# Kernel optimization log

Measured on AMD Instinct MI355X. Metric: run time of the kernel, lower is better.

## Reference

```python
import jax, jax.numpy as jnp
import numpy as np

TEMPERATURE = 0.1
LOSS_SCALE = 1.0
LAMBD = 0.5


def setup_inputs() -> dict:
    key = jax.random.key(0)
    k1, k2 = jax.random.split(key)
    B, D = 4096, 768
    predicted = jax.random.normal(k1, (B, D), dtype=jnp.float32)
    target = jax.random.normal(k2, (B, D), dtype=jnp.float32)
    return {"predicted": predicted, "target": target}


def reference(predicted, target):
    predicted = predicted.astype(jnp.float32)
    target = target.astype(jnp.float32)
    B = predicted.shape[0]

    # Pairwise L2 distances via Gram identity (avoids B x B x D intermediate):
    # ||p_i - t_j||^2 = ||p_i||^2 + ||t_j||^2 - 2 p_i . t_j
    p_sq = jnp.sum(predicted * predicted, axis=-1)  # [B]
    t_sq = jnp.sum(target * target, axis=-1)        # [B]
    cross = predicted @ target.T                    # [B, B]
    sq_dist = p_sq[:, None] + t_sq[None, :] - 2.0 * cross
    distances = jnp.sqrt(jnp.maximum(sq_dist, 0.0))  # [B, B]

    logits = -distances / TEMPERATURE
    # cross-entropy with labels = arange(B): mean of -log_softmax diagonal
    log_probs = jax.nn.log_softmax(logits, axis=-1)
    contrastive_dist_loss = -jnp.mean(jnp.diagonal(log_probs))

    # normalized L1 magnitude loss
    elementwise_l1 = jnp.sum(jnp.abs(predicted - target), axis=-1)  # [B]
    target_magnitude = jnp.sum(jnp.abs(target), axis=-1)            # [B]
    norm_factor = jax.lax.stop_gradient(target_magnitude)
    normalized_magnitude_loss = jnp.mean(elementwise_l1 / norm_factor)

    total_loss = LOSS_SCALE * (
        LAMBD * contrastive_dist_loss + (1.0 - LAMBD) * normalized_magnitude_loss
    )
    return (total_loss, contrastive_dist_loss, normalized_magnitude_loss)
```

## Files before the change

### kernel.cpp

```cpp
#include <hip/hip_runtime.h>
#include <hip/hip_bf16.h>
#include <math.h>

#define B_ROWS 4096
#define D_DIM  768

#define BM 128
#define BN 256
#define BK 32
#define NKT (D_DIM / BK)
#define NBUF 3
#define KT_STRIDE (B_ROWS * 32)
#define A_USH (BM * BK)
#define AB_USH ((BM + BN) * BK)
#define NBLK ((B_ROWS / BM) * (B_ROWS / BN))

typedef __attribute__((ext_vector_type(8))) short bf16x8;
typedef __attribute__((ext_vector_type(4))) float f32x4;

__device__ __forceinline__ unsigned short f32_to_bf16(float x) {
    unsigned int u = __float_as_uint(x);
    return (unsigned short)((u + 0x7fffu + ((u >> 16) & 1u)) >> 16);
}

__device__ __forceinline__ void async_copy16(const unsigned short* g, unsigned short* l) {
    __builtin_amdgcn_global_load_lds(
        (const __attribute__((address_space(1))) unsigned int*)g,
        (__attribute__((address_space(3))) unsigned int*)l,
        16, 0, 0);
}

__global__ void __launch_bounds__(256) rowstats_kernel(
    const float* __restrict__ P, const float* __restrict__ T,
    unsigned short* __restrict__ Pb, unsigned short* __restrict__ Tb,
    float* __restrict__ p_sq, float* __restrict__ t_sq,
    float* __restrict__ diagl, float* __restrict__ magr,
    float* __restrict__ rowsum)
{
    const int wave = threadIdx.x >> 6, lane = threadIdx.x & 63;
    const int i = blockIdx.x * 4 + wave;
    const f32x4* prow = (const f32x4*)(P + (size_t)i * D_DIM);
    const f32x4* trow = (const f32x4*)(T + (size_t)i * D_DIM);
    const int swz = (i >> 1) & 3;

    float psq = 0.f, tsq = 0.f, cr = 0.f, l1 = 0.f, tm = 0.f;
    #pragma unroll
    for (int u = 0; u < 3; ++u) {
        const int c4 = u * 64 + lane;
        f32x4 p = prow[c4], t = trow[c4];
        #pragma unroll
        for (int k = 0; k < 4; ++k) {
            psq += p[k] * p[k]; tsq += t[k] * t[k]; cr += p[k] * t[k];
            l1 += fabsf(p[k] - t[k]); tm += fabsf(t[k]);
        }
        const int kt  = c4 >> 3;
        const int cc  = (c4 >> 1) & 3;
        const int sub = c4 & 1;
        const size_t doff = (size_t)kt * KT_STRIDE + (size_t)i * 32
                          + (size_t)(((cc ^ swz) << 3) + (sub << 2));
        *(ushort4*)(Pb + doff) = make_ushort4(f32_to_bf16(p[0]), f32_to_bf16(p[1]),
                                              f32_to_bf16(p[2]), f32_to_bf16(p[3]));
        *(ushort4*)(Tb + doff) = make_ushort4(f32_to_bf16(t[0]), f32_to_bf16(t[1]),
                                              f32_to_bf16(t[2]), f32_to_bf16(t[3]));
    }
    #pragma unroll
    for (int m = 1; m < 64; m <<= 1) {
        psq += __shfl_xor(psq, m, 64);
        tsq += __shfl_xor(tsq, m, 64);
        cr  += __shfl_xor(cr,  m, 64);
        l1  += __shfl_xor(l1,  m, 64);
        tm  += __shfl_xor(tm,  m, 64);
    }
    if (lane == 0) {
        p_sq[i] = psq;
        t_sq[i] = tsq;
        float sq = fmaxf(psq + tsq - 2.0f * cr, 0.0f);
        diagl[i] = -sqrtf(sq) * 10.0f;
        magr[i]  = l1 / tm;
        rowsum[i] = 0.0f;
    }
}

__global__ void __launch_bounds__(512, 4) lse_gemm_kernel(
    const unsigned short* __restrict__ Pb, const unsigned short* __restrict__ Tb,
    const float* __restrict__ p_sq, const float* __restrict__ t_sq,
    const float* __restrict__ diagl, float* __restrict__ rowsum)
{
    __shared__ __align__(16) unsigned short S[NBUF][AB_USH];

    const int tid  = threadIdx.x;
    const int lane = tid & 63, wave = tid >> 6;

    const int flat = blockIdx.x;
    const int xcd  = flat & 7;
    const int s    = flat >> 3;
    const int ti   = ((xcd >> 1) << 3) + (s >> 3);
    const int tj   = ((xcd & 1) << 3) + (s & 7);
    const int i0   = ti * BM, j0 = tj * BN;

    const int wm = wave >> 2, wn = wave & 3;
    const int row16 = lane & 15, quad = lane >> 4;
    const int slot  = quad ^ ((row16 >> 1) & 3);

    int aoff[4], boff[4];
    #pragma unroll
    for (int mt = 0; mt < 4; ++mt)
        aoff[mt] = (wm * 64 + mt * 16 + row16) * BK + (slot << 3);
    #pragma unroll
    for (int nt = 0; nt < 4; ++nt)
        boff[nt] = A_USH + (wn * 64 + nt * 16 + row16) * BK + (slot << 3);

    const unsigned short* gp[3];
    int lb[3];
    #pragma unroll
    for (int k = 0; k < 3; ++k) {
        const int idx  = wave * 3 + k;
        const bool isB = idx >= 8;
        const int grp  = isB ? (idx - 8) : idx;
        const unsigned short* base = isB ? Tb : Pb;
        const int r0 = isB ? j0 : i0;
        gp[k] = base + (size_t)(r0 + grp * 16) * 32 + lane * 8;
        lb[k] = (isB ? A_USH : 0) + grp * 512;
    }

    f32x4 acc[4][4];
    #pragma unroll
    for (int a = 0; a < 4; ++a)
        #pragma unroll
        for (int b = 0; b < 4; ++b)
            acc[a][b] = (f32x4){0.f, 0.f, 0.f, 0.f};

    auto stage = [&](int t) {
        const size_t koff = (size_t)t * KT_STRIDE;
        unsigned short* dst = &S[t % NBUF][0];
        #pragma unroll
        for (int k = 0; k < 3; ++k) async_copy16(gp[k] + koff, dst + lb[k]);
    };
    auto compute = [&](int t) {
        const unsigned short* buf = &S[t % NBUF][0];
        bf16x8 a[4], b[4];
        #pragma unroll
        for (int mt = 0; mt < 4; ++mt) a[mt] = *(const bf16x8*)(buf + aoff[mt]);
        #pragma unroll
        for (int nt = 0; nt < 4; ++nt) b[nt] = *(const bf16x8*)(buf + boff[nt]);
        __builtin_amdgcn_s_setprio(1);
        #pragma unroll
        for (int mt = 0; mt < 4; ++mt)
            #pragma unroll
            for (int nt = 0; nt < 4; ++nt)
                acc[mt][nt] = __builtin_amdgcn_mfma_f32_16x16x32_bf16(
                    a[mt], b[nt], acc[mt][nt], 0, 0, 0);
        __builtin_amdgcn_s_setprio(0);
    };

    stage(0);
    stage(1);
    asm volatile("s_waitcnt vmcnt(3)" ::: "memory");
    __builtin_amdgcn_s_barrier();

    for (int t = 0; t < NKT - 2; ++t) {
        stage(t + 2);
        compute(t);
        asm volatile("s_waitcnt vmcnt(3)" ::: "memory");
        __builtin_amdgcn_s_barrier();
    }
    compute(NKT - 2);
    asm volatile("s_waitcnt vmcnt(0)" ::: "memory");
    __builtin_amdgcn_s_barrier();
    compute(NKT - 1);

    const float NT_LOG2E = -14.4269504089f;
    const float LOG2E    = 1.44269504089f;
    float tsq_l[4];
    #pragma unroll
    for (int nt = 0; nt < 4; ++nt)
        tsq_l[nt] = t_sq[j0 + wn * 64 + nt * 16 + row16];

    #pragma unroll
    for (int mt = 0; mt < 4; ++mt) {
        #pragma unroll
        for (int r = 0; r < 4; ++r) {
            const int i = i0 + wm * 64 + mt * 16 + quad * 4 + r;
            const float psq = p_sq[i];
            const float c0  = -diagl[i] * LOG2E;
            float sfin = 0.f;
            #pragma unroll
            for (int nt = 0; nt < 4; ++nt) {
                float c  = acc[mt][nt][r];
                float sq = fmaxf(fmaf(-2.0f, c, psq + tsq_l[nt]), 0.0f);
                float d  = sqrtf(sq);
                float y  = fmaf(d, NT_LOG2E, c0);
                sfin += exp2f(y);
            }
            #pragma unroll
            for (int m = 1; m < 16; m <<= 1) sfin += __shfl_xor(sfin, m, 64);
            if (row16 == 0) atomicAdd(&rowsum[i], sfin);
        }
    }
}

__global__ void __launch_bounds__(256) finalize_kernel(
    const float* __restrict__ rowsum, const float* __restrict__ magr,
    float* __restrict__ out)
{
    const int tid = threadIdx.x;
    double sc = 0.0, sm = 0.0;
    for (int i = tid; i < B_ROWS; i += 256) {
        sc += log((double)rowsum[i]);
        sm += (double)magr[i];
    }
    #pragma unroll
    for (int m = 1; m < 64; m <<= 1) {
        sc += __shfl_xor(sc, m, 64);
        sm += __shfl_xor(sm, m, 64);
    }
    __shared__ double red[4][2];
    const int wave = tid >> 6, lane = tid & 63;
    if (lane == 0) { red[wave][0] = sc; red[wave][1] = sm; }
    __syncthreads();
    if (tid == 0) {
        sc = red[0][0] + red[1][0] + red[2][0] + red[3][0];
        sm = red[0][1] + red[1][1] + red[2][1] + red[3][1];
        double lc = sc / (double)B_ROWS;
        double lm = sm / (double)B_ROWS;
        out[0] = (float)(0.5 * lc + 0.5 * lm);
        out[1] = (float)lc;
        out[2] = (float)lm;
    }
}

extern "C" void kernel_launch(void* const* d_in, const int* in_sizes, int n_in,
                              void* d_out, int out_size, void* d_ws, size_t ws_size,
                              hipStream_t stream) {
    const float* P = (const float*)d_in[0];
    const float* T = (const float*)d_in[1];
    float* out = (float*)d_out;

    char* ws = (char*)d_ws;
    float* rowsum = (float*)ws;               ws += B_ROWS * sizeof(float);
    float* p_sq   = (float*)ws;               ws += B_ROWS * sizeof(float);
    float* t_sq   = (float*)ws;               ws += B_ROWS * sizeof(float);
    float* diagl  = (float*)ws;               ws += B_ROWS * sizeof(float);
    float* magr   = (float*)ws;               ws += B_ROWS * sizeof(float);
    unsigned short* Pb = (unsigned short*)ws; ws += (size_t)B_ROWS * D_DIM * 2;
    unsigned short* Tb = (unsigned short*)ws;

    rowstats_kernel<<<B_ROWS / 4, 256, 0, stream>>>(
        P, T, Pb, Tb, p_sq, t_sq, diagl, magr, rowsum);
    lse_gemm_kernel<<<NBLK, 512, 0, stream>>>(
        Pb, Tb, p_sq, t_sq, diagl, rowsum);
    finalize_kernel<<<1, 256, 0, stream>>>(rowsum, magr, out);
}
```

Measured before the change: 114.9 us.

## Shrink GEMM tile to 128x128 with 4 waves and single-buffered 64-wide K steps

The fused distance/log-sum-exp GEMM moves from 128x256 tiles with 8 waves and a 3-stage async pipeline to 128x128 tiles with 4 waves. Each iteration loads two 32-wide K slices into one LDS buffer and computes both, with a barrier on each side. The block-to-XCD mapping is rearranged for the new grid. This doubles the block count and cuts LDS per block to raise occupancy, but it drops the overlap between copies and compute and doubles operand reloads per output.

Result: slower. 131.9 us (+14.8%).

```diff
diff --git a/kernel.cpp b/kernel.cpp
--- a/kernel.cpp
+++ b/kernel.cpp
@@ -6,13 +6,11 @@
 #define D_DIM  768
 
 #define BM 128
-#define BN 256
+#define BN 128
 #define BK 32
-#define NKT (D_DIM / BK)
-#define NBUF 3
+#define NKT (D_DIM / 64)
 #define KT_STRIDE (B_ROWS * 32)
-#define A_USH (BM * BK)
-#define AB_USH ((BM + BN) * BK)
+#define HALF_USH 8192
 #define NBLK ((B_ROWS / BM) * (B_ROWS / BN))
 
 typedef __attribute__((ext_vector_type(8))) short bf16x8;
@@ -81,12 +79,12 @@
     }
 }
 
-__global__ void __launch_bounds__(512, 4) lse_gemm_kernel(
+__global__ void __launch_bounds__(256) lse_gemm_kernel(
     const unsigned short* __restrict__ Pb, const unsigned short* __restrict__ Tb,
     const float* __restrict__ p_sq, const float* __restrict__ t_sq,
     const float* __restrict__ diagl, float* __restrict__ rowsum)
 {
-    __shared__ __align__(16) unsigned short S[NBUF][AB_USH];
+    __shared__ __align__(16) unsigned short S[2 * HALF_USH];
 
     const int tid  = threadIdx.x;
     const int lane = tid & 63, wave = tid >> 6;
@@ -94,11 +92,11 @@
     const int flat = blockIdx.x;
     const int xcd  = flat & 7;
     const int s    = flat >> 3;
-    const int ti   = ((xcd >> 1) << 3) + (s >> 3);
-    const int tj   = ((xcd & 1) << 3) + (s & 7);
+    const int ti   = ((xcd & 1) << 4) + (s & 15);
+    const int tj   = ((xcd >> 1) << 3) + (s >> 4);
     const int i0   = ti * BM, j0 = tj * BN;
 
-    const int wm = wave >> 2, wn = wave & 3;
+    const int wm = wave >> 1, wn = wave & 1;
     const int row16 = lane & 15, quad = lane >> 4;
     const int slot  = quad ^ ((row16 >> 1) & 3);
 
@@ -108,19 +106,19 @@
         aoff[mt] = (wm * 64 + mt * 16 + row16) * BK + (slot << 3);
     #pragma unroll
     for (int nt = 0; nt < 4; ++nt)
-        boff[nt] = A_USH + (wn * 64 + nt * 16 + row16) * BK + (slot << 3);
-
-    const unsigned short* gp[3];
-    int lb[3];
-    #pragma unroll
-    for (int k = 0; k < 3; ++k) {
-        const int idx  = wave * 3 + k;
-        const bool isB = idx >= 8;
-        const int grp  = isB ? (idx - 8) : idx;
-        const unsigned short* base = isB ? Tb : Pb;
-        const int r0 = isB ? j0 : i0;
-        gp[k] = base + (size_t)(r0 + grp * 16) * 32 + lane * 8;
-        lb[k] = (isB ? A_USH : 0) + grp * 512;
+        boff[nt] = 4096 + (wn * 64 + nt * 16 + row16) * BK + (slot << 3);
+
+    const int  sub  = wave >> 1;
+    const bool isB  = wave & 1;
+    const unsigned short* gsrc = isB ? Tb : Pb;
+    const int  r0g  = isB ? j0 : i0;
+    const unsigned short* gp[8];
+    int lb[8];
+    #pragma unroll
+    for (int k = 0; k < 8; ++k) {
+        gp[k] = gsrc + (size_t)sub * KT_STRIDE
+                     + (size_t)(r0g + k * 16) * 32 + lane * 8;
+        lb[k] = sub * HALF_USH + (isB ? 4096 : 0) + k * 512;
     }
 
     f32x4 acc[4][4];
@@ -130,44 +128,32 @@
         for (int b = 0; b < 4; ++b)
             acc[a][b] = (f32x4){0.f, 0.f, 0.f, 0.f};
 
-    auto stage = [&](int t) {
-        const size_t koff = (size_t)t * KT_STRIDE;
-        unsigned short* dst = &S[t % NBUF][0];
-        #pragma unroll
-        for (int k = 0; k < 3; ++k) async_copy16(gp[k] + koff, dst + lb[k]);
-    };
-    auto compute = [&](int t) {
-        const unsigned short* buf = &S[t % NBUF][0];
-        bf16x8 a[4], b[4];
-        #pragma unroll
-        for (int mt = 0; mt < 4; ++mt) a[mt] = *(const bf16x8*)(buf + aoff[mt]);
-        #pragma unroll
-        for (int nt = 0; nt < 4; ++nt) b[nt] = *(const bf16x8*)(buf + boff[nt]);
-        __builtin_amdgcn_s_setprio(1);
-        #pragma unroll
-        for (int mt = 0; mt < 4; ++mt)
-            #pragma unroll
-            for (int nt = 0; nt < 4; ++nt)
-                acc[mt][nt] = __builtin_amdgcn_mfma_f32_16x16x32_bf16(
-                    a[mt], b[nt], acc[mt][nt], 0, 0, 0);
-        __builtin_amdgcn_s_setprio(0);
-    };
-
-    stage(0);
-    stage(1);
-    asm volatile("s_waitcnt vmcnt(3)" ::: "memory");
-    __builtin_amdgcn_s_barrier();
-
-    for (int t = 0; t < NKT - 2; ++t) {
-        stage(t + 2);
-        compute(t);
-        asm volatile("s_waitcnt vmcnt(3)" ::: "memory");
-        __builtin_amdgcn_s_barrier();
-    }
-    compute(NKT - 2);
-    asm volatile("s_waitcnt vmcnt(0)" ::: "memory");
-    __builtin_amdgcn_s_barrier();
-    compute(NKT - 1);
+    for (int kt = 0; kt < NKT; ++kt) {
+        const size_t koff = (size_t)(2 * kt) * KT_STRIDE;
+        #pragma unroll
+        for (int k = 0; k < 8; ++k)
+            async_copy16(gp[k] + koff, &S[lb[k]]);
+        __syncthreads();
+
+        #pragma unroll
+        for (int h = 0; h < 2; ++h) {
+            const unsigned short* base = &S[h * HALF_USH];
+            bf16x8 a[4], b[4];
+            #pragma unroll
+            for (int mt = 0; mt < 4; ++mt) a[mt] = *(const bf16x8*)(base + aoff[mt]);
+            #pragma unroll
+            for (int nt = 0; nt < 4; ++nt) b[nt] = *(const bf16x8*)(base + boff[nt]);
+            __builtin_amdgcn_s_setprio(1);
+            #pragma unroll
+            for (int mt = 0; mt < 4; ++mt)
+                #pragma unroll
+                for (int nt = 0; nt < 4; ++nt)
+                    acc[mt][nt] = __builtin_amdgcn_mfma_f32_16x16x32_bf16(
+                        a[mt], b[nt], acc[mt][nt], 0, 0, 0);
+            __builtin_amdgcn_s_setprio(0);
+        }
+        __syncthreads();
+    }
 
     const float NT_LOG2E = -14.4269504089f;
     const float LOG2E    = 1.44269504089f;
@@ -247,7 +233,7 @@
 
     rowstats_kernel<<<B_ROWS / 4, 256, 0, stream>>>(
         P, T, Pb, Tb, p_sq, t_sq, diagl, magr, rowsum);
-    lse_gemm_kernel<<<NBLK, 512, 0, stream>>>(
+    lse_gemm_kernel<<<NBLK, 256, 0, stream>>>(
         Pb, Tb, p_sq, t_sq, diagl, rowsum);
     finalize_kernel<<<1, 256, 0, stream>>>(rowsum, magr, out);
 }
```
